# Kernel optimization log

Measured on AMD Instinct MI355X. Metric: run time of the kernel, lower is better.

Reference implementation:

```python
import jax, jax.numpy as jnp
import numpy as np

N = 100000      # nodes
E = 1600000     # edges
NSG2 = 20000    # subgraph2 count
NSG = 2000      # subgraph count
NG = 64         # graphs
D = 64          # hidden dim
L = 5           # conv layers


def setup_inputs() -> dict:
    key = jax.random.key(0)
    ks = jax.random.split(key, 40)
    f = lambda i, shape: (jax.random.normal(ks[i], shape, jnp.float32) * 0.05)
    inp = {
        'z': jax.random.randint(ks[0], (N, 2), 0, 100),
        'edge_index': jax.random.randint(ks[1], (2, E), 0, N),
        'node_to_subgraph2': jax.random.randint(ks[2], (N,), 0, NSG2),
        'subgraph2_to_subgraph': jax.random.randint(ks[3], (NSG2,), 0, NSG),
        'subgraph_to_graph': jax.random.randint(ks[4], (NSG,), 0, NG),
        # learned params (stacked across the 5 layers where identical shape)
        'z_emb': f(5, (L, 100, D)),
        'trans_W': f(6, (L - 1, 2 * D, D)),  # transform_before_conv, layers 1..4
        'trans_b': f(7, (L - 1, D)),
        'conv_W': f(8, (L, D, D)),           # GatedGraphConv weight (num_layers=1)
        'gru_Wih': f(9, (L, D, 3 * D)),
        'gru_bih': f(10, (L, 3 * D)),
        'gru_Whh': f(11, (L, D, 3 * D)),
        'gru_bhh': f(12, (L, 3 * D)),
        'ep_W1': f(13, (D, D)), 'ep_b1': f(14, (D,)),
        'ep_W2': f(15, (D, D)), 'ep_b2': f(16, (D,)),
        'np_W1': f(17, (D, D)), 'np_b1': f(18, (D,)),
        'np_W2': f(19, (D, D)), 'np_b2': f(20, (D,)),
        'fc1_W': f(21, (D, 32)), 'fc1_b': f(22, (32,)),
        'fc2_W': f(23, (32, 16)), 'fc2_b': f(24, (16,)),
        'fc3_W': f(25, (16, 1)), 'fc3_b': f(26, (1,)),
    }
    return inp


def _gated_conv(x, src, dst, W, Wih, bih, Whh, bhh):
    # GatedGraphConv(out=64, num_layers=1): m = aggr_add(x_j @ W), x = GRUCell(m, x)
    h = x @ W                                            # [N, D]
    m = jax.ops.segment_sum(h[src], dst, num_segments=N)  # scatter-add messages
    gi = m @ Wih + bih                                   # [N, 3D]
    gh = x @ Whh + bhh
    ir, iz, inn = jnp.split(gi, 3, axis=-1)
    hr, hz, hn = jnp.split(gh, 3, axis=-1)
    r = jax.nn.sigmoid(ir + hr)
    zg = jax.nn.sigmoid(iz + hz)
    n = jnp.tanh(inn + r * hn)
    return (1.0 - zg) * n + zg * x


def reference(z, edge_index, node_to_subgraph2, subgraph2_to_subgraph, subgraph_to_graph,
              z_emb, trans_W, trans_b, conv_W, gru_Wih, gru_bih, gru_Whh, gru_bhh,
              ep_W1, ep_b1, ep_W2, ep_b2, np_W1, np_b1, np_W2, np_b2,
              fc1_W, fc1_b, fc2_W, fc2_b, fc3_W, fc3_b):
    src, dst = edge_index[0], edge_index[1]
    x = None
    for layer in range(L):
        ze = z_emb[layer][z].sum(axis=1)  # [N,2,D] -> [N,D]
        if x is None:
            x = ze
        else:
            x = jnp.concatenate([x, ze], axis=-1) @ trans_W[layer - 1] + trans_b[layer - 1]
        x = _gated_conv(x, src, dst, conv_W[layer], gru_Wih[layer], gru_bih[layer],
                        gru_Whh[layer], gru_bhh[layer])
    # 3-level add pooling with MLPs in between
    x = jax.ops.segment_sum(x, node_to_subgraph2, num_segments=NSG2)
    x = jax.nn.relu(x @ ep_W1 + ep_b1) @ ep_W2 + ep_b2
    x = jax.ops.segment_sum(x, subgraph2_to_subgraph, num_segments=NSG)
    x = jax.nn.relu(x @ np_W1 + np_b1) @ np_W2 + np_b2
    x = jax.ops.segment_sum(x, subgraph_to_graph, num_segments=NG)
    x = jax.nn.elu(x @ fc1_W + fc1_b)
    x = jax.nn.elu(x @ fc2_W + fc2_b)
    return x @ fc3_W + fc3_b  # [NG, 1]
```

## Files before the change

kernel.cpp:

```cpp
#include <hip/hip_runtime.h>
#include <hip/hip_bf16.h>

constexpr int N    = 100000;
constexpr int E    = 1600000;
constexpr int NSG2 = 20000;
constexpr int NSG  = 2000;
constexpr int NG   = 64;
constexpr int D    = 64;
constexpr int L    = 5;

constexpr int CB    = (N + 255) / 256;
constexpr int NSTR  = 8;
constexpr int SCAP2 = 768;
constexpr int NBIN  = 48;

typedef __attribute__((ext_vector_type(8))) short short8v;
typedef __attribute__((ext_vector_type(4))) float f32x4;

__device__ __forceinline__ float sigm(float x) { return 1.0f / (1.0f + expf(-x)); }
__device__ __forceinline__ float elu(float x)  { return x > 0.0f ? x : (expf(x) - 1.0f); }

__device__ __forceinline__ unsigned short f2b(float f) {
    union { float f; unsigned u; } x; x.f = f;
    unsigned r = (x.u + 0x7FFFu + ((x.u >> 16) & 1u)) >> 16;
    return (unsigned short)r;
}
__device__ __forceinline__ float b2f(unsigned short h) {
    union { unsigned u; float f; } x; x.u = (unsigned)h << 16;
    return x.f;
}

__global__ __launch_bounds__(256) void prep_kernel(const float* __restrict__ convW,
                                                   const float* __restrict__ Wih,
                                                   float* __restrict__ WihP) {
    int idx = blockIdx.x * 256 + threadIdx.x;
    if (idx >= L * 64 * 192) return;
    int l = idx / (64 * 192);
    int rem = idx % (64 * 192);
    int i = rem / 192, j = rem % 192;
    const float* W  = convW + l * 64 * 64;
    const float* Wi = Wih  + l * 64 * 192;
    float acc = 0.0f;
    for (int t = 0; t < 64; ++t) acc = fmaf(W[i * 64 + t], Wi[t * 192 + j], acc);
    WihP[idx] = acc;
}

__global__ __launch_bounds__(256) void packg_kernel(const float* __restrict__ WihP,
                                                    const float* __restrict__ gWhh,
                                                    unsigned short* __restrict__ Wgpk) {
    int idx = blockIdx.x * 256 + threadIdx.x;
    if (idx >= L * 2 * 12 * 2 * 64) return;
    int lane = idx & 63;
    int r1 = idx >> 6;
    int t  = r1 & 1;
    int r2 = r1 >> 1;
    int nt = r2 % 12;
    int lm = r2 / 12;
    int mat = lm & 1, l = lm >> 1;
    const float* W = mat ? (gWhh + (size_t)l * 64 * 192) : (WihP + (size_t)l * 64 * 192);
    int n  = nt * 16 + (lane & 15);
    int k0 = t * 32 + (lane >> 4) * 8;
    short8v v;
#pragma unroll
    for (int j = 0; j < 8; ++j) v[j] = (short)f2b(W[(k0 + j) * 192 + n]);
    *(short8v*)(Wgpk + (size_t)idx * 8) = v;
}

__global__ __launch_bounds__(256) void packt_kernel(const float* __restrict__ tW,
                                                    unsigned short* __restrict__ tWpk) {
    int idx = blockIdx.x * 256 + threadIdx.x;
    if (idx >= (L - 1) * 4 * 4 * 64) return;
    int lane = idx & 63;
    int r1 = idx >> 6;
    int t  = r1 & 3;
    int r2 = r1 >> 2;
    int nt = r2 & 3;
    int lm = r2 >> 2;
    const float* W = tW + (size_t)lm * 128 * 64;
    int n  = nt * 16 + (lane & 15);
    int k0 = t * 32 + (lane >> 4) * 8;
    short8v v;
#pragma unroll
    for (int j = 0; j < 8; ++j) v[j] = (short)f2b(W[(k0 + j) * 64 + n]);
    *(short8v*)(tWpk + (size_t)idx * 8) = v;
}

__global__ void csrA_kernel(const int* __restrict__ src, const int* __restrict__ dst,
                            int* __restrict__ bcnt, unsigned* __restrict__ tmp) {
    int stripe = blockIdx.x & (NSTR - 1);
    for (int e = blockIdx.x * blockDim.x + threadIdx.x; e < E; e += gridDim.x * blockDim.x) {
        int d = dst[e];
        int cell = stripe * CB + (d >> 8);
        int pos = atomicAdd(&bcnt[cell * 16], 1);
        if (pos < SCAP2)
            tmp[(size_t)cell * SCAP2 + pos] = ((unsigned)(d & 255) << 17) | (unsigned)src[e];
    }
}

__global__ __launch_bounds__(256) void csrB_kernel(const unsigned* __restrict__ tmp,
                                                   const int* __restrict__ bcnt,
                                                   int* __restrict__ rowptr,
                                                   int* __restrict__ col) {
    __shared__ int hist[256];
    __shared__ int scanb[256];
    __shared__ int cur[256];
    __shared__ int scnt[NSTR];
    __shared__ int red[4];
    int b = blockIdx.x, t = threadIdx.x;
    int lane = t & 63, wid = t >> 6;

    int myb = 0;
    for (int cb = t; cb < b; cb += 256) {
        int tot = 0;
#pragma unroll
        for (int s = 0; s < NSTR; ++s) tot += min(bcnt[(s * CB + cb) * 16], SCAP2);
        myb += tot;
    }
#pragma unroll
    for (int off = 32; off > 0; off >>= 1) myb += __shfl_down(myb, off, 64);
    if (lane == 0) red[wid] = myb;
    if (t < NSTR) scnt[t] = min(bcnt[(t * CB + b) * 16], SCAP2);
    hist[t] = 0;
    __syncthreads();
    int base = red[0] + red[1] + red[2] + red[3];

    for (int s = 0; s < NSTR; ++s)
        for (int i = t; i < scnt[s]; i += 256)
            atomicAdd(&hist[tmp[((size_t)s * CB + b) * SCAP2 + i] >> 17], 1);
    __syncthreads();

    scanb[t] = hist[t];
    __syncthreads();
    for (int off = 1; off < 256; off <<= 1) {
        int v = (t >= off) ? scanb[t - off] : 0;
        __syncthreads();
        scanb[t] += v;
        __syncthreads();
    }
    int excl = scanb[t] - hist[t];
    int node = b * 256 + t;
    if (node < N) rowptr[node] = base + excl;
    if (b == CB - 1 && t == 255) rowptr[N] = base + scanb[255];
    cur[t] = base + excl;
    __syncthreads();

    for (int s = 0; s < NSTR; ++s)
        for (int i = t; i < scnt[s]; i += 256) {
            unsigned rec = tmp[((size_t)s * CB + b) * SCAP2 + i];
            int pos = atomicAdd(&cur[rec >> 17], 1);
            col[pos] = (int)(rec & 0x1FFFFu);
        }
}

__global__ __launch_bounds__(256) void degh_kernel(const int* __restrict__ rowptr,
                                                   int* __restrict__ bh) {
    __shared__ int h[NBIN];
    int b = blockIdx.x, t = threadIdx.x;
    if (t < NBIN) h[t] = 0;
    __syncthreads();
    int node = b * 256 + t;
    if (node < N) {
        int d = rowptr[node + 1] - rowptr[node];
        atomicAdd(&h[min(d, NBIN - 1)], 1);
    }
    __syncthreads();
    if (t < NBIN) bh[b * NBIN + t] = h[t];
}

__global__ __launch_bounds__(512) void degscan_par_kernel(int* __restrict__ bh,
                                                          int* __restrict__ bintot) {
    __shared__ int sh[512];
    int bin = blockIdx.x, t = threadIdx.x;
    int v = (t < CB) ? bh[t * NBIN + bin] : 0;
    sh[t] = v;
    __syncthreads();
    for (int off = 1; off < 512; off <<= 1) {
        int u = (t >= off) ? sh[t - off] : 0;
        __syncthreads();
        sh[t] += u;
        __syncthreads();
    }
    if (t < CB) bh[t * NBIN + bin] = sh[t] - v;
    if (t == 511) bintot[bin] = sh[511];
}

__global__ __launch_bounds__(64) void binbase_kernel(int* __restrict__ bintot) {
    __shared__ int sh[NBIN];
    int t = threadIdx.x;
    int v = (t < NBIN) ? bintot[t] : 0;
    if (t < NBIN) sh[t] = v;
    __syncthreads();
    if (t == 0) {
        int r = 0;
        for (int j = 0; j < NBIN; ++j) { int x = sh[j]; sh[j] = r; r += x; }
    }
    __syncthreads();
    if (t < NBIN) bintot[t] = sh[t];
}

__global__ __launch_bounds__(256) void degscat_kernel(const int* __restrict__ rowptr,
                                                      const int* __restrict__ bh,
                                                      const int* __restrict__ binbase,
                                                      int* __restrict__ perm) {
    __shared__ int cur[NBIN];
    int b = blockIdx.x, t = threadIdx.x;
    if (t < NBIN) cur[t] = bh[b * NBIN + t] + binbase[t];
    __syncthreads();
    int node = b * 256 + t;
    if (node < N) {
        int d = rowptr[node + 1] - rowptr[node];
        int pos = atomicAdd(&cur[min(d, NBIN - 1)], 1);
        perm[pos] = node;
    }
}

__global__ __launch_bounds__(256) void embed_kernel(const int* __restrict__ z,
                                                    const float* __restrict__ zemb0,
                                                    unsigned short* __restrict__ xb) {
    int idx = blockIdx.x * 256 + threadIdx.x;
    if (idx >= N * 16) return;
    int n = idx >> 4, k4 = idx & 15;
    float4 e0 = ((const float4*)(zemb0 + (size_t)z[n * 2] * 64))[k4];
    float4 e1 = ((const float4*)(zemb0 + (size_t)z[n * 2 + 1] * 64))[k4];
    ushort4 b; b.x = f2b(e0.x + e1.x); b.y = f2b(e0.y + e1.y);
    b.z = f2b(e0.z + e1.z); b.w = f2b(e0.w + e1.w);
    ((ushort4*)xb)[idx] = b;
}

template<int HAS_T>
__global__ __launch_bounds__(256, 8) void fused_kernel(const unsigned short* __restrict__ xb_in,
                                                       unsigned short* __restrict__ xb_out,
                                                       const int* __restrict__ rowptr,
                                                       const int* __restrict__ col,
                                                       const int* __restrict__ perm,
                                                       const unsigned short* __restrict__ Wgpk_l,
                                                       const float* __restrict__ bih,
                                                       const float* __restrict__ bhh,
                                                       const int* __restrict__ z,
                                                       const float* __restrict__ zemb_next,
                                                       const unsigned short* __restrict__ tWpk_next,
                                                       const float* __restrict__ tb_next,
                                                       const int* __restrict__ n2s2,
                                                       float* __restrict__ sg2) {
    __shared__ union {
        struct { unsigned short s[32][72]; unsigned short x[32][72]; } p1;
        unsigned short a[32][136];
    } u;
    int tid = threadIdx.x;
    int node0 = blockIdx.x * 32;
    int lane = tid & 63, w = tid >> 6;

    {
        int g8 = lane >> 3, cj = lane & 7;
        int nl = w * 8 + g8;
        int node = perm[node0 + nl];
        float4 ownx = ((const float4*)(xb_in + (size_t)node * 64))[cj];
        int beg = rowptr[node], end = rowptr[node + 1];
        float a[8] = {};
        const unsigned short* __restrict__ xbc = xb_in + cj * 8;
        int i = beg;
        for (; i + 8 <= end; i += 8) {
            int u0 = col[i],     u1 = col[i + 1], u2 = col[i + 2], u3 = col[i + 3];
            int u4 = col[i + 4], u5 = col[i + 5], u6 = col[i + 6], u7 = col[i + 7];
            short8v v0 = *(const short8v*)(xbc + (size_t)u0 * 64);
            short8v v1 = *(const short8v*)(xbc + (size_t)u1 * 64);
            short8v v2 = *(const short8v*)(xbc + (size_t)u2 * 64);
            short8v v3 = *(const short8v*)(xbc + (size_t)u3 * 64);
            short8v v4 = *(const short8v*)(xbc + (size_t)u4 * 64);
            short8v v5 = *(const short8v*)(xbc + (size_t)u5 * 64);
            short8v v6 = *(const short8v*)(xbc + (size_t)u6 * 64);
            short8v v7 = *(const short8v*)(xbc + (size_t)u7 * 64);
#pragma unroll
            for (int j = 0; j < 8; ++j)
                a[j] += ((b2f((unsigned short)v0[j]) + b2f((unsigned short)v1[j])) +
                         (b2f((unsigned short)v2[j]) + b2f((unsigned short)v3[j]))) +
                        ((b2f((unsigned short)v4[j]) + b2f((unsigned short)v5[j])) +
                         (b2f((unsigned short)v6[j]) + b2f((unsigned short)v7[j])));
        }
        for (; i + 4 <= end; i += 4) {
            int u0 = col[i], u1 = col[i + 1], u2 = col[i + 2], u3 = col[i + 3];
            short8v v0 = *(const short8v*)(xbc + (size_t)u0 * 64);
            short8v v1 = *(const short8v*)(xbc + (size_t)u1 * 64);
            short8v v2 = *(const short8v*)(xbc + (size_t)u2 * 64);
            short8v v3 = *(const short8v*)(xbc + (size_t)u3 * 64);
#pragma unroll
            for (int j = 0; j < 8; ++j)
                a[j] += (b2f((unsigned short)v0[j]) + b2f((unsigned short)v1[j])) +
                        (b2f((unsigned short)v2[j]) + b2f((unsigned short)v3[j]));
        }
        for (; i + 2 <= end; i += 2) {
            int u0 = col[i], u1 = col[i + 1];
            short8v v0 = *(const short8v*)(xbc + (size_t)u0 * 64);
            short8v v1 = *(const short8v*)(xbc + (size_t)u1 * 64);
#pragma unroll
            for (int j = 0; j < 8; ++j)
                a[j] += b2f((unsigned short)v0[j]) + b2f((unsigned short)v1[j]);
        }
        if (i < end) {
            short8v v = *(const short8v*)(xbc + (size_t)col[i] * 64);
#pragma unroll
            for (int j = 0; j < 8; ++j) a[j] += b2f((unsigned short)v[j]);
        }
        short8v r;
#pragma unroll
        for (int j = 0; j < 8; ++j) r[j] = (short)f2b(a[j]);
        *(short8v*)&u.p1.s[nl][cj * 8] = r;
        *(float4*)&u.p1.x[nl][cj * 8] = ownx;
    }
    __syncthreads();

    int lr = lane & 15, lg = lane >> 4;
    int ch = w * 16 + lr;
    short8v as_[2][2], ax_[2][2];
#pragma unroll
    for (int mt = 0; mt < 2; ++mt)
#pragma unroll
        for (int t = 0; t < 2; ++t) {
            int row = mt * 16 + lr, koff = t * 32 + lg * 8;
            as_[mt][t] = *(const short8v*)&u.p1.s[row][koff];
            ax_[mt][t] = *(const short8v*)&u.p1.x[row][koff];
        }
    float xres[2][4];
#pragma unroll
    for (int mt = 0; mt < 2; ++mt)
#pragma unroll
        for (int reg = 0; reg < 4; ++reg)
            xres[mt][reg] = b2f(u.p1.x[mt * 16 + lg * 4 + reg][ch]);
    if (HAS_T) __syncthreads();

    f32x4 accA[3][2] = {};
    f32x4 accB[3][2] = {};
#pragma unroll
    for (int g = 0; g < 3; ++g) {
        int nt = g * 4 + w;
#pragma unroll
        for (int t = 0; t < 2; ++t) {
            const unsigned short* pA = Wgpk_l + ((size_t)((0 * 12 + nt) * 2 + t) * 64 + lane) * 8;
            const unsigned short* pB = Wgpk_l + ((size_t)((1 * 12 + nt) * 2 + t) * 64 + lane) * 8;
            short8v bA = *(const short8v*)pA;
            short8v bB = *(const short8v*)pB;
#pragma unroll
            for (int mt = 0; mt < 2; ++mt) {
                accA[g][mt] = __builtin_amdgcn_mfma_f32_16x16x32_bf16(as_[mt][t], bA, accA[g][mt], 0, 0, 0);
                accB[g][mt] = __builtin_amdgcn_mfma_f32_16x16x32_bf16(ax_[mt][t], bB, accB[g][mt], 0, 0, 0);
            }
        }
    }

    float bi0 = bih[ch], bi1 = bih[64 + ch], bi2 = bih[128 + ch];
    float bh0 = bhh[ch], bh1 = bhh[64 + ch], bh2 = bhh[128 + ch];
    float xo[2][4];
#pragma unroll
    for (int mt = 0; mt < 2; ++mt) {
#pragma unroll
        for (int reg = 0; reg < 4; ++reg) {
            float r  = sigm(accA[0][mt][reg] + bi0 + accB[0][mt][reg] + bh0);
            float zg = sigm(accA[1][mt][reg] + bi1 + accB[1][mt][reg] + bh1);
            float nn = tanhf(accA[2][mt][reg] + bi2 + r * (accB[2][mt][reg] + bh2));
            xo[mt][reg] = (1.0f - zg) * nn + zg * xres[mt][reg];
        }
    }

    if (HAS_T == 0) {
#pragma unroll
        for (int mt = 0; mt < 2; ++mt)
#pragma unroll
            for (int reg = 0; reg < 4; ++reg) {
                int m = mt * 16 + lg * 4 + reg;
                atomicAdd(&sg2[(size_t)n2s2[perm[node0 + m]] * 64 + ch], xo[mt][reg]);
            }
        return;
    }

#pragma unroll
    for (int mt = 0; mt < 2; ++mt)
#pragma unroll
        for (int reg = 0; reg < 4; ++reg) {
            int m = mt * 16 + lg * 4 + reg;
            u.a[m][ch] = f2b(xo[mt][reg]);
        }
#pragma unroll
    for (int it = 0; it < 2; ++it) {
        int idx = it * 256 + tid;
        int n = idx >> 4, k4 = idx & 15;
        int pn = perm[node0 + n];
        int z0 = z[pn * 2], z1 = z[pn * 2 + 1];
        float4 e0 = ((const float4*)(zemb_next + (size_t)z0 * 64))[k4];
        float4 e1 = ((const float4*)(zemb_next + (size_t)z1 * 64))[k4];
        ushort4 b;
        b.x = f2b(e0.x + e1.x); b.y = f2b(e0.y + e1.y);
        b.z = f2b(e0.z + e1.z); b.w = f2b(e0.w + e1.w);
        *(ushort4*)&u.a[n][64 + k4 * 4] = b;
    }
    __syncthreads();

    f32x4 tacc[2] = {};
#pragma unroll
    for (int t = 0; t < 4; ++t) {
        const unsigned short* pB = tWpk_next + ((size_t)(w * 4 + t) * 64 + lane) * 8;
        short8v bf = *(const short8v*)pB;
#pragma unroll
        for (int mt = 0; mt < 2; ++mt) {
            int row = mt * 16 + lr, koff = t * 32 + lg * 8;
            short8v af = *(const short8v*)&u.a[row][koff];
            tacc[mt] = __builtin_amdgcn_mfma_f32_16x16x32_bf16(af, bf, tacc[mt], 0, 0, 0);
        }
    }
    float tbc = tb_next[ch];

    __shared__ unsigned short outb[32][72];
#pragma unroll
    for (int mt = 0; mt < 2; ++mt)
#pragma unroll
        for (int reg = 0; reg < 4; ++reg) {
            int m = mt * 16 + lg * 4 + reg;
            outb[m][ch] = f2b(tacc[mt][reg] + tbc);
        }
    __syncthreads();
    {
        int r = tid >> 3, q = tid & 7;
        *(float4*)(xb_out + (size_t)perm[node0 + r] * 64 + q * 8) = *(const float4*)&outb[r][q * 8];
    }
}

__global__ void pool_kernel(const float* __restrict__ in, const int* __restrict__ idx,
                            float* __restrict__ out, int rows) {
    int i = blockIdx.x * 256 + threadIdx.x;
    if (i >= rows * 64) return;
    int r = i >> 6, c = i & 63;
    atomicAdd(out + (size_t)idx[r] * 64 + c, in[i]);
}

__global__ __launch_bounds__(256) void mlp_kernel(float* __restrict__ buf,
                                                  const float* __restrict__ W1,
                                                  const float* __restrict__ b1,
                                                  const float* __restrict__ W2,
                                                  const float* __restrict__ b2) {
    __shared__ float in_t[4][64];
    __shared__ float h_t[4][64];
    int tid = threadIdx.x;
    int c = tid & 63, r = tid >> 6;
    int row0 = blockIdx.x * 4;
    in_t[r][c] = buf[(size_t)(row0 + r) * 64 + c];
    __syncthreads();
    float acc = b1[c];
    for (int k = 0; k < 64; ++k) acc = fmaf(in_t[r][k], W1[k * 64 + c], acc);
    h_t[r][c] = fmaxf(acc, 0.0f);
    __syncthreads();
    acc = b2[c];
    for (int k = 0; k < 64; ++k) acc = fmaf(h_t[r][k], W2[k * 64 + c], acc);
    buf[(size_t)(row0 + r) * 64 + c] = acc;
}

__global__ __launch_bounds__(256) void final_kernel(const float* __restrict__ g,
                                                    const float* __restrict__ fc1W, const float* __restrict__ fc1b,
                                                    const float* __restrict__ fc2W, const float* __restrict__ fc2b,
                                                    const float* __restrict__ fc3W, const float* __restrict__ fc3b,
                                                    float* __restrict__ out) {
    __shared__ float gt[64][64];
    __shared__ float h1[64][32];
    __shared__ float h2[64][16];
    int tid = threadIdx.x;
    for (int i = tid; i < 64 * 64; i += 256) gt[i >> 6][i & 63] = g[i];
    __syncthreads();
    for (int i = tid; i < 64 * 32; i += 256) {
        int r = i >> 5, c = i & 31;
        float acc = fc1b[c];
        for (int k = 0; k < 64; ++k) acc = fmaf(gt[r][k], fc1W[k * 32 + c], acc);
        h1[r][c] = elu(acc);
    }
    __syncthreads();
    for (int i = tid; i < 64 * 16; i += 256) {
        int r = i >> 4, c = i & 15;
        float acc = fc2b[c];
        for (int k = 0; k < 32; ++k) acc = fmaf(h1[r][k], fc2W[k * 16 + c], acc);
        h2[r][c] = elu(acc);
    }
    __syncthreads();
    if (tid < 64) {
        float acc = fc3b[0];
        for (int k = 0; k < 16; ++k) acc = fmaf(h2[tid][k], fc3W[k], acc);
        out[tid] = acc;
    }
}

extern "C" void kernel_launch(void* const* d_in, const int* in_sizes, int n_in,
                              void* d_out, int out_size, void* d_ws, size_t ws_size,
                              hipStream_t stream) {
    const int*   z     = (const int*)d_in[0];
    const int*   ei    = (const int*)d_in[1];
    const int*   n2s2  = (const int*)d_in[2];
    const int*   s22s  = (const int*)d_in[3];
    const int*   s2g   = (const int*)d_in[4];
    const float* z_emb = (const float*)d_in[5];
    const float* tW    = (const float*)d_in[6];
    const float* tb    = (const float*)d_in[7];
    const float* convW = (const float*)d_in[8];
    const float* gWih  = (const float*)d_in[9];
    const float* gbih  = (const float*)d_in[10];
    const float* gWhh  = (const float*)d_in[11];
    const float* gbhh  = (const float*)d_in[12];
    const float* epW1  = (const float*)d_in[13];
    const float* epb1  = (const float*)d_in[14];
    const float* epW2  = (const float*)d_in[15];
    const float* epb2  = (const float*)d_in[16];
    const float* npW1  = (const float*)d_in[17];
    const float* npb1  = (const float*)d_in[18];
    const float* npW2  = (const float*)d_in[19];
    const float* npb2  = (const float*)d_in[20];
    const float* fc1W  = (const float*)d_in[21];
    const float* fc1b  = (const float*)d_in[22];
    const float* fc2W  = (const float*)d_in[23];
    const float* fc2b  = (const float*)d_in[24];
    const float* fc3W  = (const float*)d_in[25];
    const float* fc3b  = (const float*)d_in[26];

    const int* srcp = ei;
    const int* dstp = ei + E;

    unsigned short* xbA = (unsigned short*)d_ws;
    unsigned short* xbB = xbA + (size_t)N * D;
    float*          WihP = (float*)(xbB + (size_t)N * D);
    int*            rowptr = (int*)(WihP + L * 64 * 192);
    int*            colbuf = rowptr + (N + 1);
    uintptr_t pal = (uintptr_t)(colbuf + E);
    pal = (pal + 15) & ~(uintptr_t)15;
    unsigned short* Wgpk = (unsigned short*)pal;
    unsigned short* tWpk = Wgpk + (size_t)L * 2 * 12 * 2 * 64 * 8;
    uintptr_t pal2 = (uintptr_t)(tWpk + (size_t)(L - 1) * 4 * 4 * 64 * 8);
    pal2 = (pal2 + 15) & ~(uintptr_t)15;
    unsigned* tmp  = (unsigned*)pal2;
    int*      bcnt = (int*)(tmp + (size_t)CB * NSTR * SCAP2);
    int*      perm = bcnt + (size_t)CB * NSTR * 16;
    int*      bh   = perm + N;
    int*      bintot = bh + (size_t)CB * NBIN;
    float*    sg2  = (float*)(bintot + NBIN);
    float*    sg   = sg2 + (size_t)NSG2 * D;
    float*    gbuf = sg + (size_t)NSG * D;

    hipMemsetAsync(bcnt, 0, (size_t)CB * NSTR * 16 * sizeof(int), stream);
    hipMemsetAsync(sg2, 0, (size_t)(NSG2 + NSG + NG) * D * sizeof(float), stream);

    prep_kernel<<<(L * 64 * 192 + 255) / 256, 256, 0, stream>>>(convW, gWih, WihP);
    packg_kernel<<<(L * 2 * 12 * 2 * 64 + 255) / 256, 256, 0, stream>>>(WihP, gWhh, Wgpk);
    packt_kernel<<<((L - 1) * 4 * 4 * 64 + 255) / 256, 256, 0, stream>>>(tW, tWpk);

    csrA_kernel<<<4096, 256, 0, stream>>>(srcp, dstp, bcnt, tmp);
    csrB_kernel<<<CB, 256, 0, stream>>>(tmp, bcnt, rowptr, colbuf);

    degh_kernel<<<CB, 256, 0, stream>>>(rowptr, bh);
    degscan_par_kernel<<<NBIN, 512, 0, stream>>>(bh, bintot);
    binbase_kernel<<<1, 64, 0, stream>>>(bintot);
    degscat_kernel<<<CB, 256, 0, stream>>>(rowptr, bh, bintot, perm);

    embed_kernel<<<(N * 16 + 255) / 256, 256, 0, stream>>>(z, z_emb, xbA);

    for (int l = 0; l < L; ++l) {
        const unsigned short* xin = (l & 1) ? xbB : xbA;
        unsigned short*       xout = (l & 1) ? xbA : xbB;
        if (l < L - 1) {
            fused_kernel<1><<<N / 32, 256, 0, stream>>>(
                xin, xout, rowptr, colbuf, perm,
                Wgpk + (size_t)l * 2 * 12 * 2 * 64 * 8,
                gbih + (size_t)l * 192, gbhh + (size_t)l * 192,
                z, z_emb + (size_t)(l + 1) * 100 * 64,
                tWpk + (size_t)l * 4 * 4 * 64 * 8, tb + (size_t)l * 64,
                nullptr, nullptr);
        } else {
            fused_kernel<0><<<N / 32, 256, 0, stream>>>(
                xin, nullptr, rowptr, colbuf, perm,
                Wgpk + (size_t)l * 2 * 12 * 2 * 64 * 8,
                gbih + (size_t)l * 192, gbhh + (size_t)l * 192,
                z, z_emb, tWpk, tb,
                n2s2, sg2);
        }
    }

    mlp_kernel<<<NSG2 / 4, 256, 0, stream>>>(sg2, epW1, epb1, epW2, epb2);
    pool_kernel<<<(NSG2 * D + 255) / 256, 256, 0, stream>>>(sg2, s22s, sg, NSG2);
    mlp_kernel<<<NSG / 4, 256, 0, stream>>>(sg, npW1, npb1, npW2, npb2);
    pool_kernel<<<(NSG * D + 255) / 256, 256, 0, stream>>>(sg, s2g, gbuf, NSG);
    final_kernel<<<1, 256, 0, stream>>>(gbuf, fc1W, fc1b, fc2W, fc2b, fc3W, fc3b, (float*)d_out);
}
```

Before: 462.4 us.

## Split node features into two 32-channel planes for cache-friendlier gathers

Stores the bf16 node feature matrix as two planes of 32 channels (64 bytes per node row each) instead of one 128-byte row. The neighbour aggregation now gathers each plane in a separate pass, so each pass touches a smaller working set that fits cache better. It also retunes NSTR/SCAP2 and drops the occupancy hint from launch_bounds. The cost is rereading the column indices twice and issuing narrower 8-byte loads.

```diff
diff --git a/kernel.cpp b/kernel.cpp
--- a/kernel.cpp
+++ b/kernel.cpp
@@ -10,8 +10,8 @@
 constexpr int L    = 5;
 
 constexpr int CB    = (N + 255) / 256;
-constexpr int NSTR  = 8;
-constexpr int SCAP2 = 768;
+constexpr int NSTR  = 16;
+constexpr int SCAP2 = 512;
 constexpr int NBIN  = 48;
 
 typedef __attribute__((ext_vector_type(8))) short short8v;
@@ -220,28 +220,29 @@
     int idx = blockIdx.x * 256 + threadIdx.x;
     if (idx >= N * 16) return;
     int n = idx >> 4, k4 = idx & 15;
+    int p = k4 >> 3, c4 = k4 & 7;
     float4 e0 = ((const float4*)(zemb0 + (size_t)z[n * 2] * 64))[k4];
     float4 e1 = ((const float4*)(zemb0 + (size_t)z[n * 2 + 1] * 64))[k4];
     ushort4 b; b.x = f2b(e0.x + e1.x); b.y = f2b(e0.y + e1.y);
     b.z = f2b(e0.z + e1.z); b.w = f2b(e0.w + e1.w);
-    ((ushort4*)xb)[idx] = b;
+    *(ushort4*)(xb + (size_t)p * N * 32 + (size_t)n * 32 + c4 * 4) = b;
 }
 
 template<int HAS_T>
-__global__ __launch_bounds__(256, 8) void fused_kernel(const unsigned short* __restrict__ xb_in,
-                                                       unsigned short* __restrict__ xb_out,
-                                                       const int* __restrict__ rowptr,
-                                                       const int* __restrict__ col,
-                                                       const int* __restrict__ perm,
-                                                       const unsigned short* __restrict__ Wgpk_l,
-                                                       const float* __restrict__ bih,
-                                                       const float* __restrict__ bhh,
-                                                       const int* __restrict__ z,
-                                                       const float* __restrict__ zemb_next,
-                                                       const unsigned short* __restrict__ tWpk_next,
-                                                       const float* __restrict__ tb_next,
-                                                       const int* __restrict__ n2s2,
-                                                       float* __restrict__ sg2) {
+__global__ __launch_bounds__(256) void fused_kernel(const unsigned short* __restrict__ xb_in,
+                                                    unsigned short* __restrict__ xb_out,
+                                                    const int* __restrict__ rowptr,
+                                                    const int* __restrict__ col,
+                                                    const int* __restrict__ perm,
+                                                    const unsigned short* __restrict__ Wgpk_l,
+                                                    const float* __restrict__ bih,
+                                                    const float* __restrict__ bhh,
+                                                    const int* __restrict__ z,
+                                                    const float* __restrict__ zemb_next,
+                                                    const unsigned short* __restrict__ tWpk_next,
+                                                    const float* __restrict__ tb_next,
+                                                    const int* __restrict__ n2s2,
+                                                    float* __restrict__ sg2) {
     __shared__ union {
         struct { unsigned short s[32][72]; unsigned short x[32][72]; } p1;
         unsigned short a[32][136];
@@ -254,58 +255,61 @@
         int g8 = lane >> 3, cj = lane & 7;
         int nl = w * 8 + g8;
         int node = perm[node0 + nl];
-        float4 ownx = ((const float4*)(xb_in + (size_t)node * 64))[cj];
         int beg = rowptr[node], end = rowptr[node + 1];
-        float a[8] = {};
-        const unsigned short* __restrict__ xbc = xb_in + cj * 8;
-        int i = beg;
-        for (; i + 8 <= end; i += 8) {
-            int u0 = col[i],     u1 = col[i + 1], u2 = col[i + 2], u3 = col[i + 3];
-            int u4 = col[i + 4], u5 = col[i + 5], u6 = col[i + 6], u7 = col[i + 7];
-            short8v v0 = *(const short8v*)(xbc + (size_t)u0 * 64);
-            short8v v1 = *(const short8v*)(xbc + (size_t)u1 * 64);
-            short8v v2 = *(const short8v*)(xbc + (size_t)u2 * 64);
-            short8v v3 = *(const short8v*)(xbc + (size_t)u3 * 64);
-            short8v v4 = *(const short8v*)(xbc + (size_t)u4 * 64);
-            short8v v5 = *(const short8v*)(xbc + (size_t)u5 * 64);
-            short8v v6 = *(const short8v*)(xbc + (size_t)u6 * 64);
-            short8v v7 = *(const short8v*)(xbc + (size_t)u7 * 64);
-#pragma unroll
-            for (int j = 0; j < 8; ++j)
-                a[j] += ((b2f((unsigned short)v0[j]) + b2f((unsigned short)v1[j])) +
-                         (b2f((unsigned short)v2[j]) + b2f((unsigned short)v3[j]))) +
-                        ((b2f((unsigned short)v4[j]) + b2f((unsigned short)v5[j])) +
-                         (b2f((unsigned short)v6[j]) + b2f((unsigned short)v7[j])));
-        }
-        for (; i + 4 <= end; i += 4) {
-            int u0 = col[i], u1 = col[i + 1], u2 = col[i + 2], u3 = col[i + 3];
-            short8v v0 = *(const short8v*)(xbc + (size_t)u0 * 64);
-            short8v v1 = *(const short8v*)(xbc + (size_t)u1 * 64);
-            short8v v2 = *(const short8v*)(xbc + (size_t)u2 * 64);
-            short8v v3 = *(const short8v*)(xbc + (size_t)u3 * 64);
-#pragma unroll
-            for (int j = 0; j < 8; ++j)
-                a[j] += (b2f((unsigned short)v0[j]) + b2f((unsigned short)v1[j])) +
-                        (b2f((unsigned short)v2[j]) + b2f((unsigned short)v3[j]));
-        }
-        for (; i + 2 <= end; i += 2) {
-            int u0 = col[i], u1 = col[i + 1];
-            short8v v0 = *(const short8v*)(xbc + (size_t)u0 * 64);
-            short8v v1 = *(const short8v*)(xbc + (size_t)u1 * 64);
-#pragma unroll
-            for (int j = 0; j < 8; ++j)
-                a[j] += b2f((unsigned short)v0[j]) + b2f((unsigned short)v1[j]);
-        }
-        if (i < end) {
-            short8v v = *(const short8v*)(xbc + (size_t)col[i] * 64);
-#pragma unroll
-            for (int j = 0; j < 8; ++j) a[j] += b2f((unsigned short)v[j]);
-        }
-        short8v r;
-#pragma unroll
-        for (int j = 0; j < 8; ++j) r[j] = (short)f2b(a[j]);
-        *(short8v*)&u.p1.s[nl][cj * 8] = r;
-        *(float4*)&u.p1.x[nl][cj * 8] = ownx;
+#pragma unroll
+        for (int p = 0; p < 2; ++p) {
+            const unsigned short* __restrict__ xbp = xb_in + (size_t)p * N * 32 + cj * 4;
+            ushort4 ownx = *(const ushort4*)(xbp + (size_t)node * 32);
+            float a0 = 0.f, a1 = 0.f, a2 = 0.f, a3 = 0.f;
+            int i = beg;
+            for (; i + 8 <= end; i += 8) {
+                int u0 = col[i],     u1 = col[i + 1], u2 = col[i + 2], u3 = col[i + 3];
+                int u4 = col[i + 4], u5 = col[i + 5], u6 = col[i + 6], u7 = col[i + 7];
+                ushort4 v0 = *(const ushort4*)(xbp + (size_t)u0 * 32);
+                ushort4 v1 = *(const ushort4*)(xbp + (size_t)u1 * 32);
+                ushort4 v2 = *(const ushort4*)(xbp + (size_t)u2 * 32);
+                ushort4 v3 = *(const ushort4*)(xbp + (size_t)u3 * 32);
+                ushort4 v4 = *(const ushort4*)(xbp + (size_t)u4 * 32);
+                ushort4 v5 = *(const ushort4*)(xbp + (size_t)u5 * 32);
+                ushort4 v6 = *(const ushort4*)(xbp + (size_t)u6 * 32);
+                ushort4 v7 = *(const ushort4*)(xbp + (size_t)u7 * 32);
+                a0 += ((b2f(v0.x) + b2f(v1.x)) + (b2f(v2.x) + b2f(v3.x))) +
+                      ((b2f(v4.x) + b2f(v5.x)) + (b2f(v6.x) + b2f(v7.x)));
+                a1 += ((b2f(v0.y) + b2f(v1.y)) + (b2f(v2.y) + b2f(v3.y))) +
+                      ((b2f(v4.y) + b2f(v5.y)) + (b2f(v6.y) + b2f(v7.y)));
+                a2 += ((b2f(v0.z) + b2f(v1.z)) + (b2f(v2.z) + b2f(v3.z))) +
+                      ((b2f(v4.z) + b2f(v5.z)) + (b2f(v6.z) + b2f(v7.z)));
+                a3 += ((b2f(v0.w) + b2f(v1.w)) + (b2f(v2.w) + b2f(v3.w))) +
+                      ((b2f(v4.w) + b2f(v5.w)) + (b2f(v6.w) + b2f(v7.w)));
+            }
+            for (; i + 4 <= end; i += 4) {
+                int u0 = col[i], u1 = col[i + 1], u2 = col[i + 2], u3 = col[i + 3];
+                ushort4 v0 = *(const ushort4*)(xbp + (size_t)u0 * 32);
+                ushort4 v1 = *(const ushort4*)(xbp + (size_t)u1 * 32);
+                ushort4 v2 = *(const ushort4*)(xbp + (size_t)u2 * 32);
+                ushort4 v3 = *(const ushort4*)(xbp + (size_t)u3 * 32);
+                a0 += (b2f(v0.x) + b2f(v1.x)) + (b2f(v2.x) + b2f(v3.x));
+                a1 += (b2f(v0.y) + b2f(v1.y)) + (b2f(v2.y) + b2f(v3.y));
+                a2 += (b2f(v0.z) + b2f(v1.z)) + (b2f(v2.z) + b2f(v3.z));
+                a3 += (b2f(v0.w) + b2f(v1.w)) + (b2f(v2.w) + b2f(v3.w));
+            }
+            for (; i + 2 <= end; i += 2) {
+                int u0 = col[i], u1 = col[i + 1];
+                ushort4 v0 = *(const ushort4*)(xbp + (size_t)u0 * 32);
+                ushort4 v1 = *(const ushort4*)(xbp + (size_t)u1 * 32);
+                a0 += b2f(v0.x) + b2f(v1.x);
+                a1 += b2f(v0.y) + b2f(v1.y);
+                a2 += b2f(v0.z) + b2f(v1.z);
+                a3 += b2f(v0.w) + b2f(v1.w);
+            }
+            if (i < end) {
+                ushort4 v = *(const ushort4*)(xbp + (size_t)col[i] * 32);
+                a0 += b2f(v.x); a1 += b2f(v.y); a2 += b2f(v.z); a3 += b2f(v.w);
+            }
+            ushort4 r; r.x = f2b(a0); r.y = f2b(a1); r.z = f2b(a2); r.w = f2b(a3);
+            *(ushort4*)&u.p1.s[nl][p * 32 + cj * 4] = r;
+            *(ushort4*)&u.p1.x[nl][p * 32 + cj * 4] = ownx;
+        }
     }
     __syncthreads();
 
@@ -419,7 +423,10 @@
     __syncthreads();
     {
         int r = tid >> 3, q = tid & 7;
-        *(float4*)(xb_out + (size_t)perm[node0 + r] * 64 + q * 8) = *(const float4*)&outb[r][q * 8];
+        int p = q >> 2, c4 = q & 3;
+        int pn = perm[node0 + r];
+        *(float4*)(xb_out + (size_t)p * N * 32 + (size_t)pn * 32 + c4 * 8) =
+            *(const float4*)&outb[r][p * 32 + c4 * 8];
     }
 }
 
```

Result: slower. 539.3 us (+16.6%).

## Relabel nodes into degree-sorted order to drop per-layer perm indirection

Applied to the files above, without the earlier changes.

Nodes are renumbered into the degree-sorted permutation once up front. An inverse permutation is built, CSR column indices are relabelled, and per-node row ranges, z pairs and subgraph ids are gathered into permuted arrays. The fused layer kernels then index nodes directly, which removes the perm lookups and makes the x loads and stores coalesced. The change also alters the CSR bucketing constants and drops the launch_bounds occupancy hint, at the cost of several extra setup kernels.

```diff
diff --git a/kernel.cpp b/kernel.cpp
--- a/kernel.cpp
+++ b/kernel.cpp
@@ -10,8 +10,8 @@
 constexpr int L    = 5;
 
 constexpr int CB    = (N + 255) / 256;
-constexpr int NSTR  = 8;
-constexpr int SCAP2 = 768;
+constexpr int NSTR  = 16;
+constexpr int SCAP2 = 512;
 constexpr int NBIN  = 48;
 
 typedef __attribute__((ext_vector_type(8))) short short8v;
@@ -214,34 +214,66 @@
     }
 }
 
-__global__ __launch_bounds__(256) void embed_kernel(const int* __restrict__ z,
+__global__ __launch_bounds__(256) void inv_kernel(const int* __restrict__ perm,
+                                                  int* __restrict__ inv) {
+    int i = blockIdx.x * 256 + threadIdx.x;
+    if (i < N) inv[perm[i]] = i;
+}
+
+__global__ void relabel_kernel(int* __restrict__ col, const int* __restrict__ inv,
+                               const int* __restrict__ rowptrN) {
+    int total = rowptrN[0];
+    for (int e = blockIdx.x * blockDim.x + threadIdx.x; e < total; e += gridDim.x * blockDim.x)
+        col[e] = inv[col[e]];
+}
+
+__global__ __launch_bounds__(256) void rowrange_kernel(const int* __restrict__ rowptr,
+                                                       const int* __restrict__ perm,
+                                                       const int* __restrict__ z,
+                                                       const int* __restrict__ n2s2,
+                                                       int* __restrict__ rb,
+                                                       int* __restrict__ re,
+                                                       int* __restrict__ n2s2p,
+                                                       int2* __restrict__ zp) {
+    int i = blockIdx.x * 256 + threadIdx.x;
+    if (i >= N) return;
+    int pn = perm[i];
+    rb[i] = rowptr[pn];
+    re[i] = rowptr[pn + 1];
+    n2s2p[i] = n2s2[pn];
+    int2 zz; zz.x = z[pn * 2]; zz.y = z[pn * 2 + 1];
+    zp[i] = zz;
+}
+
+__global__ __launch_bounds__(256) void embed_kernel(const int2* __restrict__ zp,
                                                     const float* __restrict__ zemb0,
                                                     unsigned short* __restrict__ xb) {
     int idx = blockIdx.x * 256 + threadIdx.x;
     if (idx >= N * 16) return;
     int n = idx >> 4, k4 = idx & 15;
-    float4 e0 = ((const float4*)(zemb0 + (size_t)z[n * 2] * 64))[k4];
-    float4 e1 = ((const float4*)(zemb0 + (size_t)z[n * 2 + 1] * 64))[k4];
+    int2 zz = zp[n];
+    float4 e0 = ((const float4*)(zemb0 + (size_t)zz.x * 64))[k4];
+    float4 e1 = ((const float4*)(zemb0 + (size_t)zz.y * 64))[k4];
     ushort4 b; b.x = f2b(e0.x + e1.x); b.y = f2b(e0.y + e1.y);
     b.z = f2b(e0.z + e1.z); b.w = f2b(e0.w + e1.w);
     ((ushort4*)xb)[idx] = b;
 }
 
 template<int HAS_T>
-__global__ __launch_bounds__(256, 8) void fused_kernel(const unsigned short* __restrict__ xb_in,
-                                                       unsigned short* __restrict__ xb_out,
-                                                       const int* __restrict__ rowptr,
-                                                       const int* __restrict__ col,
-                                                       const int* __restrict__ perm,
-                                                       const unsigned short* __restrict__ Wgpk_l,
-                                                       const float* __restrict__ bih,
-                                                       const float* __restrict__ bhh,
-                                                       const int* __restrict__ z,
-                                                       const float* __restrict__ zemb_next,
-                                                       const unsigned short* __restrict__ tWpk_next,
-                                                       const float* __restrict__ tb_next,
-                                                       const int* __restrict__ n2s2,
-                                                       float* __restrict__ sg2) {
+__global__ __launch_bounds__(256) void fused_kernel(const unsigned short* __restrict__ xb_in,
+                                                    unsigned short* __restrict__ xb_out,
+                                                    const int* __restrict__ rb,
+                                                    const int* __restrict__ re,
+                                                    const int* __restrict__ col,
+                                                    const unsigned short* __restrict__ Wgpk_l,
+                                                    const float* __restrict__ bih,
+                                                    const float* __restrict__ bhh,
+                                                    const int2* __restrict__ zp,
+                                                    const float* __restrict__ zemb_next,
+                                                    const unsigned short* __restrict__ tWpk_next,
+                                                    const float* __restrict__ tb_next,
+                                                    const int* __restrict__ n2s2p,
+                                                    float* __restrict__ sg2) {
     __shared__ union {
         struct { unsigned short s[32][72]; unsigned short x[32][72]; } p1;
         unsigned short a[32][136];
@@ -253,9 +285,9 @@
     {
         int g8 = lane >> 3, cj = lane & 7;
         int nl = w * 8 + g8;
-        int node = perm[node0 + nl];
+        int node = node0 + nl;
         float4 ownx = ((const float4*)(xb_in + (size_t)node * 64))[cj];
-        int beg = rowptr[node], end = rowptr[node + 1];
+        int beg = rb[node], end = re[node];
         float a[8] = {};
         const unsigned short* __restrict__ xbc = xb_in + cj * 8;
         int i = beg;
@@ -367,7 +399,7 @@
 #pragma unroll
             for (int reg = 0; reg < 4; ++reg) {
                 int m = mt * 16 + lg * 4 + reg;
-                atomicAdd(&sg2[(size_t)n2s2[perm[node0 + m]] * 64 + ch], xo[mt][reg]);
+                atomicAdd(&sg2[(size_t)n2s2p[node0 + m] * 64 + ch], xo[mt][reg]);
             }
         return;
     }
@@ -383,10 +415,9 @@
     for (int it = 0; it < 2; ++it) {
         int idx = it * 256 + tid;
         int n = idx >> 4, k4 = idx & 15;
-        int pn = perm[node0 + n];
-        int z0 = z[pn * 2], z1 = z[pn * 2 + 1];
-        float4 e0 = ((const float4*)(zemb_next + (size_t)z0 * 64))[k4];
-        float4 e1 = ((const float4*)(zemb_next + (size_t)z1 * 64))[k4];
+        int2 zz = zp[node0 + n];
+        float4 e0 = ((const float4*)(zemb_next + (size_t)zz.x * 64))[k4];
+        float4 e1 = ((const float4*)(zemb_next + (size_t)zz.y * 64))[k4];
         ushort4 b;
         b.x = f2b(e0.x + e1.x); b.y = f2b(e0.y + e1.y);
         b.z = f2b(e0.z + e1.z); b.w = f2b(e0.w + e1.w);
@@ -419,7 +450,7 @@
     __syncthreads();
     {
         int r = tid >> 3, q = tid & 7;
-        *(float4*)(xb_out + (size_t)perm[node0 + r] * 64 + q * 8) = *(const float4*)&outb[r][q * 8];
+        *(float4*)(xb_out + (size_t)(node0 + r) * 64 + q * 8) = *(const float4*)&outb[r][q * 8];
     }
 }
 
@@ -534,7 +565,12 @@
     int*      perm = bcnt + (size_t)CB * NSTR * 16;
     int*      bh   = perm + N;
     int*      bintot = bh + (size_t)CB * NBIN;
-    float*    sg2  = (float*)(bintot + NBIN);
+    int*      inv  = bintot + NBIN;
+    int*      rb   = inv + N;
+    int*      re   = rb + N;
+    int*      n2s2p = re + N;
+    int2*     zp   = (int2*)(n2s2p + N);
+    float*    sg2  = (float*)(zp + N);
     float*    sg   = sg2 + (size_t)NSG2 * D;
     float*    gbuf = sg + (size_t)NSG * D;
 
@@ -553,26 +589,30 @@
     binbase_kernel<<<1, 64, 0, stream>>>(bintot);
     degscat_kernel<<<CB, 256, 0, stream>>>(rowptr, bh, bintot, perm);
 
-    embed_kernel<<<(N * 16 + 255) / 256, 256, 0, stream>>>(z, z_emb, xbA);
+    inv_kernel<<<(N + 255) / 256, 256, 0, stream>>>(perm, inv);
+    relabel_kernel<<<2048, 256, 0, stream>>>(colbuf, inv, rowptr + N);
+    rowrange_kernel<<<(N + 255) / 256, 256, 0, stream>>>(rowptr, perm, z, n2s2, rb, re, n2s2p, zp);
+
+    embed_kernel<<<(N * 16 + 255) / 256, 256, 0, stream>>>(zp, z_emb, xbA);
 
     for (int l = 0; l < L; ++l) {
         const unsigned short* xin = (l & 1) ? xbB : xbA;
         unsigned short*       xout = (l & 1) ? xbA : xbB;
         if (l < L - 1) {
             fused_kernel<1><<<N / 32, 256, 0, stream>>>(
-                xin, xout, rowptr, colbuf, perm,
+                xin, xout, rb, re, colbuf,
                 Wgpk + (size_t)l * 2 * 12 * 2 * 64 * 8,
                 gbih + (size_t)l * 192, gbhh + (size_t)l * 192,
-                z, z_emb + (size_t)(l + 1) * 100 * 64,
+                zp, z_emb + (size_t)(l + 1) * 100 * 64,
                 tWpk + (size_t)l * 4 * 4 * 64 * 8, tb + (size_t)l * 64,
                 nullptr, nullptr);
         } else {
             fused_kernel<0><<<N / 32, 256, 0, stream>>>(
-                xin, nullptr, rowptr, colbuf, perm,
+                xin, nullptr, rb, re, colbuf,
                 Wgpk + (size_t)l * 2 * 12 * 2 * 64 * 8,
                 gbih + (size_t)l * 192, gbhh + (size_t)l * 192,
-                z, z_emb, tWpk, tb,
-                n2s2, sg2);
+                zp, z_emb, tWpk, tb,
+                n2s2p, sg2);
         }
     }
 
```

Result: no change. 464.9 us (+0.5%).
